# Kernel optimization log

Measured on AMD Instinct MI355X. Metric: run time of the kernel, lower is better.

Reference implementation:

```python
import jax, jax.numpy as jnp
import numpy as np

KNN = 11  # self.knn in VoronoiBaseNN


def setup_inputs() -> dict:
    key = jax.random.key(0)
    k1, k2 = jax.random.split(key)
    points = jax.random.normal(k1, (2, 50000, 3), dtype=jnp.float32)   # GT surface samples
    spoints = jax.random.normal(k2, (2, 4000, 3), dtype=jnp.float32)   # Voronoi generators
    return {"points": points, "spoints": spoints}


def reference(points, spoints):
    # Pairwise squared distances: [B, N, M]
    d2 = ((points[:, :, None, :] - spoints[:, None, :, :]) ** 2).sum(-1)
    # KNN smallest, sorted ascending (torch.topk(largest=False, sorted=True))
    _, idx = jax.lax.top_k(-d2, KNN)            # idx: [B, N, KNN]
    # Gather the KNN generator coordinates: [B, N, KNN, 3]
    gathered = jax.vmap(lambda sp, i: sp[i])(spoints, idx)
    inside = gathered[:, :, 0, :]               # closest cell center [B, N, 3]
    point_to_center = points - inside           # [B, N, 3]
    # Voronoi edge vectors to the other KNN-1 neighbors: [B, N, KNN-1, 3]
    voronoi_edge = gathered[:, :, 1:, :] - inside[:, :, None, :]
    edge_l = jnp.sqrt((voronoi_edge ** 2).sum(-1))                      # [B, N, KNN-1]
    vector_length = (point_to_center[:, :, None, :] * voronoi_edge).sum(-1) / edge_l
    sq_dist = (vector_length - edge_l / 2.0) ** 2
    return sq_dist.min(-1)                      # [B, N]
```

## Files before the change

kernel.cpp:

```cpp
#include <hip/hip_runtime.h>
#include <math.h>

#define NPTS  50000
#define NSP   4000
#define NGRP  1000
#define NW    8
#define QW    (NGRP / NW)
#define KNN   11
#define BIG   3.4e38f
#define SEGCAP 128
#define SEGPAD 8
#define SEGSTR (SEGCAP + SEGPAD)
#define GRIDC 32
#define NKEY  65536

#define MED3(a,b,c) __builtin_amdgcn_fmed3f((a),(b),(c))

__device__ unsigned g_hist[NKEY];
__device__ float4   g_sorted[2 * NPTS];

static __device__ __forceinline__ unsigned spread5(unsigned v) {
    return (v & 1u) | ((v & 2u) << 2) | ((v & 4u) << 4) |
           ((v & 8u) << 6) | ((v & 16u) << 8);
}

static __device__ __forceinline__ unsigned cell_key(int b, float x, float y, float z) {
    int gx = (int)floorf((x + 4.0f) * 4.0f);
    int gy = (int)floorf((y + 4.0f) * 4.0f);
    int gz = (int)floorf((z + 4.0f) * 4.0f);
    gx = min(max(gx, 0), GRIDC - 1);
    gy = min(max(gy, 0), GRIDC - 1);
    gz = min(max(gz, 0), GRIDC - 1);
    unsigned m = spread5((unsigned)gx) | (spread5((unsigned)gy) << 1) |
                 (spread5((unsigned)gz) << 2);
    return ((unsigned)b << 15) | m;
}

__global__ void k_zero() {
    int t = blockIdx.x * 256 + threadIdx.x;
    if (t < NKEY) g_hist[t] = 0u;
}

__global__ void k_hist(const float* __restrict__ pts) {
    int n = blockIdx.x * 256 + threadIdx.x;
    if (n >= 2 * NPTS) return;
    const float* p = pts + (size_t)n * 3;
    int b = (n >= NPTS) ? 1 : 0;
    atomicAdd(&g_hist[cell_key(b, p[0], p[1], p[2])], 1u);
}

__global__ void k_scan() {
    __shared__ unsigned part[1024];
    const int t = threadIdx.x;
    const unsigned base = (unsigned)blockIdx.x * 32768u + (unsigned)t * 32u;
    unsigned s = 0;
#pragma unroll
    for (int j = 0; j < 32; ++j) s += g_hist[base + j];
    part[t] = s;
    __syncthreads();
    for (int off = 1; off < 1024; off <<= 1) {
        unsigned v = (t >= off) ? part[t - off] : 0u;
        __syncthreads();
        part[t] += v;
        __syncthreads();
    }
    unsigned run = (unsigned)blockIdx.x * (unsigned)NPTS + part[t] - s;
#pragma unroll
    for (int j = 0; j < 32; ++j) {
        unsigned h = g_hist[base + j];
        g_hist[base + j] = run;
        run += h;
    }
}

__global__ void k_scatter(const float* __restrict__ pts) {
    int n = blockIdx.x * 256 + threadIdx.x;
    if (n >= 2 * NPTS) return;
    const float* p = pts + (size_t)n * 3;
    int b = (n >= NPTS) ? 1 : 0;
    float x = p[0], y = p[1], z = p[2];
    unsigned dst = atomicAdd(&g_hist[cell_key(b, x, y, z)], 1u);
    if (dst < 2u * NPTS)
        g_sorted[dst] = make_float4(x, y, z, __uint_as_float((unsigned)(n - b * NPTS)));
}

static __device__ __forceinline__ float wred_min(float v) {
#pragma unroll
    for (int off = 32; off > 0; off >>= 1) v = fminf(v, __shfl_xor(v, off, 64));
    return v;
}
static __device__ __forceinline__ float wred_max(float v) {
#pragma unroll
    for (int off = 32; off > 0; off >>= 1) v = fmaxf(v, __shfl_xor(v, off, 64));
    return v;
}

__global__ __launch_bounds__(512, 6) void voronoi_kernel(
    const float* __restrict__ spts,
    float* __restrict__ out)
{
    __shared__ float4 sl[NW * SEGSTR];
    __shared__ float  lds_d[NW][64][13];
    __shared__ int    lds_i[NW][64];
    __shared__ float  lds_b[NW][64];
    __shared__ float  lds_m[NW];

    const int b    = blockIdx.y;
    const int lane = threadIdx.x & 63;
    const int wq   = threadIdx.x >> 6;
    int pi = blockIdx.x * 64 + lane;
    const bool valid = (pi < NPTS);
    if (!valid) pi = NPTS - 1;

    const float4 P = g_sorted[(size_t)b * NPTS + pi];
    const float px = P.x, py = P.y, pz = P.z;
    const unsigned orig = __float_as_uint(P.w);

    const float mnx = wred_min(px), mxx = wred_max(px);
    const float mny = wred_min(py), mxy = wred_max(py);
    const float mnz = wred_min(pz), mxz = wred_max(pz);
    const float ccx = 0.5f * (mnx + mxx);
    const float ccy = 0.5f * (mny + mxy);
    const float ccz = 0.5f * (mnz + mxz);
    const float R = sqrtf(wred_max(
        fmaf(px - ccx, px - ccx, fmaf(py - ccy, py - ccy, (pz - ccz) * (pz - ccz)))));

    const float4* __restrict__ spq = (const float4*)(spts + (size_t)b * NSP * 3);
    const int g0 = wq * QW, g1 = g0 + QW;

    float myMin = BIG;
    for (int k0 = g0; k0 < g1; k0 += 64) {
        const int g  = k0 + lane;
        const int gc = (g < g1) ? g : (g1 - 1);
        const float4 q0 = spq[3 * gc + 0];
        const float4 q1 = spq[3 * gc + 1];
        const float4 q2 = spq[3 * gc + 2];
        float dx = q0.x - ccx, dy = q0.y - ccy, dz = q0.z - ccz;
        float md = fmaf(dx, dx, fmaf(dy, dy, dz * dz));
        dx = q0.w - ccx; dy = q1.x - ccy; dz = q1.y - ccz;
        md = fminf(md, fmaf(dx, dx, fmaf(dy, dy, dz * dz)));
        dx = q1.z - ccx; dy = q1.w - ccy; dz = q2.x - ccz;
        md = fminf(md, fmaf(dx, dx, fmaf(dy, dy, dz * dz)));
        dx = q2.y - ccx; dy = q2.z - ccy; dz = q2.w - ccz;
        md = fminf(md, fmaf(dx, dx, fmaf(dy, dy, dz * dz)));
        if (g < g1) myMin = fminf(myMin, md);
    }
    float vv = myMin, m11 = 0.0f;
#pragma unroll
    for (int t = 0; t < KNN; ++t) {
        m11 = wred_min(vv);
        vv = (vv == m11) ? BIG : vv;
    }
    if (lane == 0) lds_m[wq] = m11;
    __syncthreads();
    float m11g = BIG;
#pragma unroll
    for (int q = 0; q < NW; ++q) m11g = fminf(m11g, lds_m[q]);
    const float Trad = sqrtf(m11g) + R;
    const float T = Trad * Trad * 1.0004f + 1e-12f;

#define ADM(sx, sy, sz) \
    (fmaf(MED3((sx), mnx, mxx) - (sx), MED3((sx), mnx, mxx) - (sx), \
     fmaf(MED3((sy), mny, mxy) - (sy), MED3((sy), mny, mxy) - (sy), \
          (MED3((sz), mnz, mxz) - (sz)) * (MED3((sz), mnz, mxz) - (sz)))) <= T)

    const int segbase = wq * SEGSTR;
    unsigned cnt = 0;

    auto padseg = [&]() {
        if (lane < SEGPAD)
            sl[segbase + (int)cnt + lane] =
                make_float4(1e18f, 1e18f, 1e18f, __uint_as_float(0x7fffffffu));
    };

#define PUSH(sx, sy, sz, ok, idx, CONSUME) { \
        if (cnt > (unsigned)(SEGCAP - 64)) {                 \
            padseg(); CONSUME(cnt); cnt = 0; of = true; \
        } \
        const unsigned long long msk = __ballot(ok); \
        if (ok) { \
            const unsigned pos = cnt + \
                __builtin_amdgcn_mbcnt_hi((unsigned)(msk >> 32), \
                    __builtin_amdgcn_mbcnt_lo((unsigned)msk, 0u)); \
            sl[segbase + (int)pos] = \
                make_float4((sx), (sy), (sz), __uint_as_float((unsigned)(idx))); \
        } \
        cnt += (unsigned)__popcll(msk); }

#define RUN_BUILD(CONSUME, ofvar) { \
        ofvar = false; bool& of = ofvar; cnt = 0; \
        for (int k0 = g0; k0 < g1; k0 += 64) { \
            const int g  = k0 + lane; \
            const int gc = (g < g1) ? g : (g1 - 1); \
            const bool in = (g < g1); \
            const float4 q0 = spq[3 * gc + 0]; \
            const float4 q1 = spq[3 * gc + 1]; \
            const float4 q2 = spq[3 * gc + 2]; \
            const bool a0 = in && ADM(q0.x, q0.y, q0.z); \
            const bool a1 = in && ADM(q0.w, q1.x, q1.y); \
            const bool a2 = in && ADM(q1.z, q1.w, q2.x); \
            const bool a3 = in && ADM(q2.y, q2.z, q2.w); \
            PUSH(q0.x, q0.y, q0.z, a0, 4 * gc + 0, CONSUME); \
            PUSH(q0.w, q1.x, q1.y, a1, 4 * gc + 1, CONSUME); \
            PUSH(q1.z, q1.w, q2.x, a2, 4 * gc + 2, CONSUME); \
            PUSH(q2.y, q2.z, q2.w, a3, 4 * gc + 3, CONSUME); \
        } \
        padseg(); CONSUME(cnt); }

    float d0 = BIG, d1 = BIG, d2 = BIG, d3 = BIG, d4 = BIG, d5 = BIG,
          d6 = BIG, d7 = BIG, d8 = BIG, d9 = BIG, d10 = BIG;
    int i0 = 0x7fffffff;

#define CHAIN(nd, jj) { \
        if (__ballot((nd) < d10)) { \
            d10 = MED3(d9, d10, (nd)); \
            d9  = MED3(d8, d9,  (nd)); \
            d8  = MED3(d7, d8,  (nd)); \
            d7  = MED3(d6, d7,  (nd)); \
            d6  = MED3(d5, d6,  (nd)); \
            d5  = MED3(d4, d5,  (nd)); \
            d4  = MED3(d3, d4,  (nd)); \
            d3  = MED3(d2, d3,  (nd)); \
            d2  = MED3(d1, d2,  (nd)); \
            d1  = MED3(d0, d1,  (nd)); \
            i0  = ((nd) < d0) ? (jj) : i0; \
            d0  = fminf(d0, (nd)); \
        } }
#define CANDA(c) { \
        const float dx = px - (c).x, dy = py - (c).y, dz = pz - (c).z; \
        const float nd = fmaf(dx, dx, fmaf(dy, dy, dz * dz)); \
        const int jj = (int)__float_as_uint((c).w); \
        CHAIN(nd, jj); }

    auto chainA = [&](unsigned n) {
        if (n == 0u) return;
        float4 e0 = sl[segbase + 0], e1 = sl[segbase + 1],
               e2 = sl[segbase + 2], e3 = sl[segbase + 3];
        for (unsigned k = 0; k < n; k += 4) {
            const float4 n0 = sl[segbase + (int)k + 4];
            const float4 n1 = sl[segbase + (int)k + 5];
            const float4 n2 = sl[segbase + (int)k + 6];
            const float4 n3 = sl[segbase + (int)k + 7];
            CANDA(e0); CANDA(e1); CANDA(e2); CANDA(e3);
            e0 = n0; e1 = n1; e2 = n2; e3 = n3;
        }
    };

    bool ovfA;
    RUN_BUILD(chainA, ovfA);
    const unsigned cntA = cnt;

    lds_d[wq][lane][0]  = d0;  lds_d[wq][lane][1]  = d1;
    lds_d[wq][lane][2]  = d2;  lds_d[wq][lane][3]  = d3;
    lds_d[wq][lane][4]  = d4;  lds_d[wq][lane][5]  = d5;
    lds_d[wq][lane][6]  = d6;  lds_d[wq][lane][7]  = d7;
    lds_d[wq][lane][8]  = d8;  lds_d[wq][lane][9]  = d9;
    lds_d[wq][lane][10] = d10;
    lds_i[wq][lane] = i0;
    __syncthreads();

    float gb = BIG; int gi = 0x7fffffff;
#pragma unroll
    for (int q = 0; q < NW; ++q) {
        const float dq = lds_d[q][lane][0];
        const int   iq = lds_i[q][lane];
        const bool take = (dq < gb) || (dq == gb && iq < gi);
        gb = take ? dq : gb;
        gi = take ? iq : gi;
    }
#define INS(v) { \
        d10 = MED3(d9, d10, (v)); \
        d9  = MED3(d8, d9,  (v)); \
        d8  = MED3(d7, d8,  (v)); \
        d7  = MED3(d6, d7,  (v)); \
        d6  = MED3(d5, d6,  (v)); \
        d5  = MED3(d4, d5,  (v)); \
        d4  = MED3(d3, d4,  (v)); \
        d3  = MED3(d2, d3,  (v)); \
        d2  = MED3(d1, d2,  (v)); \
        d1  = MED3(d0, d1,  (v)); \
        d0  = fminf(d0, (v)); }
#pragma unroll
    for (int q = 0; q < NW; ++q) {
        if (q == wq) continue;
#pragma unroll
        for (int k = 0; k < 11; ++k) {
            const float v = lds_d[q][lane][k];
            if (!__ballot(v < d10)) break;
            INS(v);
        }
    }
    const float d10g = d10;
    const int   i0g  = gi;

    const float* ip = spts + (size_t)b * NSP * 3 + (size_t)(unsigned)i0g * 3;
    const float ix = ip[0], iy = ip[1], iz = ip[2];
    const float vx = px - ix, vy = py - iy, vz = pz - iz;
    float best = BIG;

#define CANDB(c) { \
        const float dx = px - (c).x, dy = py - (c).y, dz = pz - (c).z; \
        const float nd = fmaf(dx, dx, fmaf(dy, dy, dz * dz)); \
        const int jj = (int)__float_as_uint((c).w); \
        const bool adm = (nd <= d10g) && (jj != i0g); \
        if (__ballot(adm)) { \
            const float ex = (c).x - ix, ey = (c).y - iy, ez = (c).z - iz; \
            const float ee = fmaf(ex, ex, fmaf(ey, ey, ez * ez)); \
            const float dt = fmaf(vx, ex, fmaf(vy, ey, vz * ez)); \
            const float u  = fmaf(-0.5f, ee, dt); \
            const float t2 = u * u * __builtin_amdgcn_rcpf(ee); \
            best = adm ? fminf(best, t2) : best; \
        } }

    auto scanB = [&](unsigned n) {
        if (n == 0u) return;
        float4 e0 = sl[segbase + 0], e1 = sl[segbase + 1],
               e2 = sl[segbase + 2], e3 = sl[segbase + 3];
        for (unsigned k = 0; k < n; k += 4) {
            const float4 n0 = sl[segbase + (int)k + 4];
            const float4 n1 = sl[segbase + (int)k + 5];
            const float4 n2 = sl[segbase + (int)k + 6];
            const float4 n3 = sl[segbase + (int)k + 7];
            CANDB(e0); CANDB(e1); CANDB(e2); CANDB(e3);
            e0 = n0; e1 = n1; e2 = n2; e3 = n3;
        }
    };

    if (!ovfA) {
        scanB(cntA);
    } else {
        bool ovfB;
        RUN_BUILD(scanB, ovfB);
        (void)ovfB;
    }

    lds_b[wq][lane] = best;
    __syncthreads();
    if (wq == 0) {
        float m = lds_b[0][lane];
#pragma unroll
        for (int q = 1; q < NW; ++q) m = fminf(m, lds_b[q][lane]);
        if (valid) out[(size_t)b * NPTS + orig] = m;
    }
}

extern "C" void kernel_launch(void* const* d_in, const int* in_sizes, int n_in,
                              void* d_out, int out_size, void* d_ws, size_t ws_size,
                              hipStream_t stream) {
    (void)in_sizes; (void)n_in; (void)d_ws; (void)ws_size; (void)out_size;
    const float* pts  = (const float*)d_in[0];
    const float* spts = (const float*)d_in[1];
    float* out = (float*)d_out;

    k_zero   <<<dim3(NKEY / 256),            dim3(256),  0, stream>>>();
    k_hist   <<<dim3((2 * NPTS + 255)/256),  dim3(256),  0, stream>>>(pts);
    k_scan   <<<dim3(2),                     dim3(1024), 0, stream>>>();
    k_scatter<<<dim3((2 * NPTS + 255)/256),  dim3(256),  0, stream>>>(pts);
    voronoi_kernel<<<dim3((NPTS + 63)/64, 2), dim3(512), 0, stream>>>(spts, out);
}
```

Baseline: 258.3 us.

## Fuse preprocessing into one cooperative kernel and retune voronoi occupancy

Replaces the four preprocessing launches (zero, histogram, scan, scatter) with a single cooperative kernel that uses grid syncs, with the old launches kept as a fallback. It also shrinks the segment cache and per-lane distance buffer so the voronoi kernel can target more blocks per CU, and permutes the block-to-group mapping to spread heavy spatial groups across the launch. The aim is to remove launch gaps and improve occupancy and load balance. The risks are grid-sync overhead, the smaller SEGCAP forcing more segment refills, and register pressure under the tighter launch bounds.

```diff
diff --git a/kernel.cpp b/kernel.cpp
--- a/kernel.cpp
+++ b/kernel.cpp
@@ -1,4 +1,5 @@
 #include <hip/hip_runtime.h>
+#include <hip/hip_cooperative_groups.h>
 #include <math.h>
 
 #define NPTS  50000
@@ -8,15 +9,17 @@
 #define QW    (NGRP / NW)
 #define KNN   11
 #define BIG   3.4e38f
-#define SEGCAP 128
+#define SEGCAP 96
 #define SEGPAD 8
 #define SEGSTR (SEGCAP + SEGPAD)
 #define GRIDC 32
 #define NKEY  65536
+#define NGB   ((NPTS + 63) / 64)
 
 #define MED3(a,b,c) __builtin_amdgcn_fmed3f((a),(b),(c))
 
 __device__ unsigned g_hist[NKEY];
+__device__ unsigned g_bsum[256];
 __device__ float4   g_sorted[2 * NPTS];
 
 static __device__ __forceinline__ unsigned spread5(unsigned v) {
@@ -36,11 +39,68 @@
     return ((unsigned)b << 15) | m;
 }
 
+__global__ void k_pre(const float* __restrict__ pts) {
+    cooperative_groups::grid_group gg = cooperative_groups::this_grid();
+    __shared__ unsigned sc[256];
+    const int t   = threadIdx.x;
+    const int bb  = blockIdx.x;
+    const int tid = bb * 256 + t;
+
+    g_hist[tid] = 0u;
+    gg.sync();
+
+    for (int n = tid; n < 2 * NPTS; n += NKEY) {
+        const float* p = pts + (size_t)n * 3;
+        atomicAdd(&g_hist[cell_key(n >= NPTS, p[0], p[1], p[2])], 1u);
+    }
+    gg.sync();
+
+    const unsigned v = g_hist[tid];
+    sc[t] = v;
+    __syncthreads();
+    for (int off = 1; off < 256; off <<= 1) {
+        const unsigned u = (t >= off) ? sc[t - off] : 0u;
+        __syncthreads();
+        sc[t] += u;
+        __syncthreads();
+    }
+    const unsigned excl = sc[t] - v;
+    if (t == 255) g_bsum[bb] = sc[255];
+    gg.sync();
+
+    if (bb == 0) {
+        const unsigned s = g_bsum[t];
+        __syncthreads();
+        sc[t] = s;
+        __syncthreads();
+        for (int off = 1; off < 256; off <<= 1) {
+            const unsigned u = (t >= off) ? sc[t - off] : 0u;
+            __syncthreads();
+            sc[t] += u;
+            __syncthreads();
+        }
+        g_bsum[t] = sc[t] - s;
+    }
+    gg.sync();
+
+    g_hist[tid] = excl + g_bsum[bb];
+    gg.sync();
+
+    for (int n = tid; n < 2 * NPTS; n += NKEY) {
+        const float* p = pts + (size_t)n * 3;
+        const int bq = (n >= NPTS);
+        const float x = p[0], y = p[1], z = p[2];
+        const unsigned dst = atomicAdd(&g_hist[cell_key(bq, x, y, z)], 1u);
+        if (dst < 2u * NPTS)
+            g_sorted[dst] = make_float4(x, y, z,
+                                        __uint_as_float((unsigned)(n - bq * NPTS)));
+    }
+}
+
 __global__ void k_zero() {
     int t = blockIdx.x * 256 + threadIdx.x;
     if (t < NKEY) g_hist[t] = 0u;
 }
-
 __global__ void k_hist(const float* __restrict__ pts) {
     int n = blockIdx.x * 256 + threadIdx.x;
     if (n >= 2 * NPTS) return;
@@ -48,7 +108,6 @@
     int b = (n >= NPTS) ? 1 : 0;
     atomicAdd(&g_hist[cell_key(b, p[0], p[1], p[2])], 1u);
 }
-
 __global__ void k_scan() {
     __shared__ unsigned part[1024];
     const int t = threadIdx.x;
@@ -72,7 +131,6 @@
         run += h;
     }
 }
-
 __global__ void k_scatter(const float* __restrict__ pts) {
     int n = blockIdx.x * 256 + threadIdx.x;
     if (n >= 2 * NPTS) return;
@@ -95,12 +153,12 @@
     return v;
 }
 
-__global__ __launch_bounds__(512, 6) void voronoi_kernel(
+__global__ __launch_bounds__(512, 8) void voronoi_kernel(
     const float* __restrict__ spts,
     float* __restrict__ out)
 {
     __shared__ float4 sl[NW * SEGSTR];
-    __shared__ float  lds_d[NW][64][13];
+    __shared__ float  lds_d[NW][64][11];
     __shared__ int    lds_i[NW][64];
     __shared__ float  lds_b[NW][64];
     __shared__ float  lds_m[NW];
@@ -108,7 +166,8 @@
     const int b    = blockIdx.y;
     const int lane = threadIdx.x & 63;
     const int wq   = threadIdx.x >> 6;
-    int pi = blockIdx.x * 64 + lane;
+    const int grp  = (int)(((unsigned)blockIdx.x * 401u) % (unsigned)NGB);
+    int pi = grp * 64 + lane;
     const bool valid = (pi < NPTS);
     if (!valid) pi = NPTS - 1;
 
@@ -352,9 +411,15 @@
     const float* spts = (const float*)d_in[1];
     float* out = (float*)d_out;
 
-    k_zero   <<<dim3(NKEY / 256),            dim3(256),  0, stream>>>();
-    k_hist   <<<dim3((2 * NPTS + 255)/256),  dim3(256),  0, stream>>>(pts);
-    k_scan   <<<dim3(2),                     dim3(1024), 0, stream>>>();
-    k_scatter<<<dim3((2 * NPTS + 255)/256),  dim3(256),  0, stream>>>(pts);
-    voronoi_kernel<<<dim3((NPTS + 63)/64, 2), dim3(512), 0, stream>>>(spts, out);
-}
+    const float* pts_arg = pts;
+    void* args[] = { (void*)&pts_arg };
+    hipError_t ce = hipLaunchCooperativeKernel((const void*)k_pre,
+                                               dim3(256), dim3(256), args, 0, stream);
+    if (ce != hipSuccess) {
+        k_zero   <<<dim3(NKEY / 256),            dim3(256),  0, stream>>>();
+        k_hist   <<<dim3((2 * NPTS + 255)/256),  dim3(256),  0, stream>>>(pts);
+        k_scan   <<<dim3(2),                     dim3(1024), 0, stream>>>();
+        k_scatter<<<dim3((2 * NPTS + 255)/256),  dim3(256),  0, stream>>>(pts);
+    }
+    voronoi_kernel<<<dim3(NGB, 2), dim3(512), 0, stream>>>(spts, out);
+}
```

Result: slower. 393.4 us (+52.3%).
